# Optimization experiments

Measured on AMD Instinct MI355X. Metric: run time of the kernel, lower is better.

Reference implementation:

```python
import jax, jax.numpy as jnp
import numpy as np


def setup_inputs() -> dict:
    key = jax.random.key(0)
    k1, k2 = jax.random.split(key)
    B, T, D = 16, 4096, 512
    x = jax.random.normal(k1, (B, T, D), dtype=jnp.float32)
    alpha = jax.random.normal(k2, (1, 1, D), dtype=jnp.float32)  # raw param, pre-sigmoid
    return {"x": x, "alpha": alpha}


def reference(x, alpha):
    # s_0 = x_0 ; s_t = a * x_t + (1 - a) * s_{t-1}, a = sigmoid(alpha)
    a = jax.nn.sigmoid(alpha[0, 0, :])  # (D,)
    one_minus_a = 1.0 - a

    def step(prev, xt):  # prev, xt: (B, D)
        cur = a * xt + one_minus_a * prev
        return cur, cur

    x_t = jnp.swapaxes(x, 0, 1)  # (T, B, D)
    init = x_t[0]
    _, rest = jax.lax.scan(step, init, x_t[1:])  # (T-1, B, D)
    states = jnp.concatenate([x_t[:1], rest], axis=0)  # (T, B, D)
    return jnp.swapaxes(states, 0, 1)  # (B, T, D)
```

## Files before the change

kernel.cpp:

```cpp
#include <hip/hip_runtime.h>
#include <math.h>

#define BB 16
#define TT 4096
#define DD 512
#define D4 128

constexpr int CC = 256;
constexpr int LL = TT / CC;

typedef float floatx4 __attribute__((ext_vector_type(4)));

__device__ __forceinline__ float sigmf(float v) {
    return 1.0f / (1.0f + expf(-v));
}

__global__ __launch_bounds__(256) void es_chunk_ends(
    const float* __restrict__ x, const float* __restrict__ alpha,
    float* __restrict__ ends)
{
    const int c   = blockIdx.x;
    const int tid = threadIdx.x;
    const int b   = (blockIdx.y << 1) + (tid >> 7);
    const int d4  = tid & 127;

    const float4* xp = reinterpret_cast<const float4*>(x)
                     + ((size_t)b * TT + (size_t)c * LL) * D4 + d4;

    float4 v[LL];
    #pragma unroll
    for (int i = 0; i < LL; ++i) v[i] = xp[(size_t)i * D4];

    const float4 al = reinterpret_cast<const float4*>(alpha)[d4];
    const float ax = sigmf(al.x), ay = sigmf(al.y), az = sigmf(al.z), aw = sigmf(al.w);
    const float fx = 1.0f - ax, fy = 1.0f - ay, fz = 1.0f - az, fw = 1.0f - aw;

    float4 s;
    if (c == 0) {
        s = v[0];
    } else {
        s.x = s.y = s.z = s.w = 0.0f;
    }

    #pragma unroll
    for (int i = 0; i < LL; ++i) {
        s.x = fmaf(ax, v[i].x, fx * s.x);
        s.y = fmaf(ay, v[i].y, fy * s.y);
        s.z = fmaf(az, v[i].z, fz * s.z);
        s.w = fmaf(aw, v[i].w, fw * s.w);
    }

    reinterpret_cast<float4*>(ends)[((size_t)b * CC + c) * D4 + d4] = s;
}

__global__ __launch_bounds__(256) void es_carry_scan(
    float* __restrict__ ends, const float* __restrict__ alpha)
{
    const int g  = blockIdx.x * 256 + threadIdx.x;
    const int b  = g >> 7;
    const int d4 = g & 127;

    const float4 al = reinterpret_cast<const float4*>(alpha)[d4];
    const float ax = sigmf(al.x), ay = sigmf(al.y), az = sigmf(al.z), aw = sigmf(al.w);
    float4 fL;
    fL.x = powf(1.0f - ax, (float)LL);
    fL.y = powf(1.0f - ay, (float)LL);
    fL.z = powf(1.0f - az, (float)LL);
    fL.w = powf(1.0f - aw, (float)LL);

    float4* e = reinterpret_cast<float4*>(ends) + (size_t)b * CC * D4 + d4;

    constexpr int P = 16;
    float4 buf[P];
    #pragma unroll
    for (int j = 0; j < P; ++j) buf[j] = e[(size_t)(1 + j) * D4];

    float4 S = e[0];
    int c = 1;
    while (c + P <= CC) {
        #pragma unroll
        for (int j = 0; j < P; ++j) {
            const float4 v = buf[j];
            const int pf = c + P;
            if (pf < CC) buf[j] = e[(size_t)pf * D4];
            S.x = fmaf(fL.x, S.x, v.x);
            S.y = fmaf(fL.y, S.y, v.y);
            S.z = fmaf(fL.z, S.z, v.z);
            S.w = fmaf(fL.w, S.w, v.w);
            e[(size_t)c * D4] = S;
            ++c;
        }
    }
    for (int j = 0; c < CC; ++c, ++j) {
        const float4 v = buf[j];
        S.x = fmaf(fL.x, S.x, v.x);
        S.y = fmaf(fL.y, S.y, v.y);
        S.z = fmaf(fL.z, S.z, v.z);
        S.w = fmaf(fL.w, S.w, v.w);
        e[(size_t)c * D4] = S;
    }
}

__global__ __launch_bounds__(256) void es_final(
    const float* __restrict__ x, const float* __restrict__ alpha,
    const float* __restrict__ carries, float* __restrict__ out)
{
    const int c   = blockIdx.x;
    const int tid = threadIdx.x;
    const int b   = (blockIdx.y << 1) + (tid >> 7);
    const int d4  = tid & 127;

    float4 s;
    if (c != 0) {
        s = reinterpret_cast<const float4*>(carries)[((size_t)b * CC + (c - 1)) * D4 + d4];
    }

    const size_t base = ((size_t)b * TT + (size_t)c * LL) * D4 + d4;
    const float4* xp = reinterpret_cast<const float4*>(x) + base;
    floatx4*      op = reinterpret_cast<floatx4*>(out) + base;

    float4 v[LL];
    #pragma unroll
    for (int i = 0; i < LL; ++i) v[i] = xp[(size_t)i * D4];

    const float4 al = reinterpret_cast<const float4*>(alpha)[d4];
    const float ax = sigmf(al.x), ay = sigmf(al.y), az = sigmf(al.z), aw = sigmf(al.w);
    const float fx = 1.0f - ax, fy = 1.0f - ay, fz = 1.0f - az, fw = 1.0f - aw;

    if (c == 0) s = v[0];

    #pragma unroll
    for (int i = 0; i < LL; ++i) {
        s.x = fmaf(ax, v[i].x, fx * s.x);
        s.y = fmaf(ay, v[i].y, fy * s.y);
        s.z = fmaf(az, v[i].z, fz * s.z);
        s.w = fmaf(aw, v[i].w, fw * s.w);
        floatx4 sv = { s.x, s.y, s.z, s.w };
        __builtin_nontemporal_store(sv, op + (size_t)i * D4);
    }
}

__global__ __launch_bounds__(256) void es_serial(
    const float* __restrict__ x, const float* __restrict__ alpha,
    float* __restrict__ out)
{
    const int g  = blockIdx.x * 256 + threadIdx.x;
    const int b  = g >> 7;
    const int d4 = g & 127;

    const float4 al = reinterpret_cast<const float4*>(alpha)[d4];
    const float ax = sigmf(al.x), ay = sigmf(al.y), az = sigmf(al.z), aw = sigmf(al.w);
    const float fx = 1.0f - ax, fy = 1.0f - ay, fz = 1.0f - az, fw = 1.0f - aw;

    const float4* xp = reinterpret_cast<const float4*>(x) + (size_t)b * TT * D4 + d4;
    float4*       op = reinterpret_cast<float4*>(out) + (size_t)b * TT * D4 + d4;

    float4 s = xp[0];
    #pragma unroll 4
    for (int t = 0; t < TT; ++t) {
        const float4 v = xp[(size_t)t * D4];
        s.x = fmaf(ax, v.x, fx * s.x);
        s.y = fmaf(ay, v.y, fy * s.y);
        s.z = fmaf(az, v.z, fz * s.z);
        s.w = fmaf(aw, v.w, fw * s.w);
        op[(size_t)t * D4] = s;
    }
}

extern "C" void kernel_launch(void* const* d_in, const int* in_sizes, int n_in,
                              void* d_out, int out_size, void* d_ws, size_t ws_size,
                              hipStream_t stream)
{
    const float* x     = (const float*)d_in[0];
    const float* alpha = (const float*)d_in[1];
    float*       out   = (float*)d_out;

    const size_t need = (size_t)BB * CC * DD * sizeof(float);
    if (ws_size < need) {
        es_serial<<<dim3(8), 256, 0, stream>>>(x, alpha, out);
        return;
    }

    float* ends = (float*)d_ws;
    es_chunk_ends<<<dim3(CC, BB / 2), 256, 0, stream>>>(x, alpha, ends);
    es_carry_scan<<<dim3(8), 256, 0, stream>>>(ends, alpha);
    es_final<<<dim3(CC, BB / 2), 256, 0, stream>>>(x, alpha, ends, out);
}
```

Measured before the change: 270.8 us.

## Fuse three-pass chunked scan into one cooperative kernel with grid syncs

```diff
diff --git a/kernel.cpp b/kernel.cpp
--- a/kernel.cpp
+++ b/kernel.cpp
@@ -1,18 +1,141 @@
 #include <hip/hip_runtime.h>
+#include <hip/hip_cooperative_groups.h>
 #include <math.h>
+
+namespace cg = cooperative_groups;
 
 #define BB 16
 #define TT 4096
 #define DD 512
 #define D4 128
 
-constexpr int CC = 256;
-constexpr int LL = TT / CC;
+constexpr int CCF = 128;
+constexpr int LLF = TT / CCF;
+constexpr int CC  = 256;
+constexpr int LL  = TT / CC;
 
 typedef float floatx4 __attribute__((ext_vector_type(4)));
 
 __device__ __forceinline__ float sigmf(float v) {
     return 1.0f / (1.0f + expf(-v));
+}
+
+__global__ __launch_bounds__(256, 4) void es_fused(
+    const float* __restrict__ x, const float* __restrict__ alpha,
+    float* __restrict__ ends, float* __restrict__ out)
+{
+    const int tid = threadIdx.x;
+    const int c   = blockIdx.x & (CCF - 1);
+    const int b   = ((blockIdx.x >> 7) << 1) + (tid >> 7);
+    const int d4  = tid & 127;
+
+    const float4 al = reinterpret_cast<const float4*>(alpha)[d4];
+    const float ax = sigmf(al.x), ay = sigmf(al.y), az = sigmf(al.z), aw = sigmf(al.w);
+    const float fx = 1.0f - ax, fy = 1.0f - ay, fz = 1.0f - az, fw = 1.0f - aw;
+
+    const size_t base = ((size_t)b * TT + (size_t)c * LLF) * D4 + d4;
+
+    {
+        const float4* xp = reinterpret_cast<const float4*>(x) + base;
+        constexpr int W = 8;
+        float4 w[W];
+        #pragma unroll
+        for (int j = 0; j < W; ++j) w[j] = xp[(size_t)j * D4];
+
+        float4 s;
+        if (c == 0) s = w[0];
+        else        { s.x = s.y = s.z = s.w = 0.0f; }
+
+        #pragma unroll
+        for (int i = 0; i < LLF; ++i) {
+            const float4 v = w[i & (W - 1)];
+            if (i + W < LLF) w[i & (W - 1)] = xp[(size_t)(i + W) * D4];
+            s.x = fmaf(ax, v.x, fx * s.x);
+            s.y = fmaf(ay, v.y, fy * s.y);
+            s.z = fmaf(az, v.z, fz * s.z);
+            s.w = fmaf(aw, v.w, fw * s.w);
+        }
+        reinterpret_cast<float4*>(ends)[((size_t)b * CCF + c) * D4 + d4] = s;
+    }
+
+    cg::this_grid().sync();
+
+    {
+        const int g = blockIdx.x * 256 + tid;
+        if (g < BB * D4) {
+            const int sb  = g >> 7;
+            const int sd4 = g & 127;
+            const float4 sal = reinterpret_cast<const float4*>(alpha)[sd4];
+            float4 fL;
+            fL.x = powf(1.0f - sigmf(sal.x), (float)LLF);
+            fL.y = powf(1.0f - sigmf(sal.y), (float)LLF);
+            fL.z = powf(1.0f - sigmf(sal.z), (float)LLF);
+            fL.w = powf(1.0f - sigmf(sal.w), (float)LLF);
+
+            float4* e = reinterpret_cast<float4*>(ends) + (size_t)sb * CCF * D4 + sd4;
+
+            constexpr int P = 8;
+            float4 buf[P];
+            #pragma unroll
+            for (int j = 0; j < P; ++j) buf[j] = e[(size_t)(1 + j) * D4];
+
+            float4 S = e[0];
+            int cc = 1;
+            while (cc + P <= CCF) {
+                #pragma unroll
+                for (int j = 0; j < P; ++j) {
+                    const float4 v = buf[j];
+                    const int pf = cc + P;
+                    if (pf < CCF) buf[j] = e[(size_t)pf * D4];
+                    S.x = fmaf(fL.x, S.x, v.x);
+                    S.y = fmaf(fL.y, S.y, v.y);
+                    S.z = fmaf(fL.z, S.z, v.z);
+                    S.w = fmaf(fL.w, S.w, v.w);
+                    e[(size_t)cc * D4] = S;
+                    ++cc;
+                }
+            }
+            for (int j = 0; cc < CCF; ++cc, ++j) {
+                const float4 v = buf[j];
+                S.x = fmaf(fL.x, S.x, v.x);
+                S.y = fmaf(fL.y, S.y, v.y);
+                S.z = fmaf(fL.z, S.z, v.z);
+                S.w = fmaf(fL.w, S.w, v.w);
+                e[(size_t)cc * D4] = S;
+            }
+        }
+    }
+
+    cg::this_grid().sync();
+
+    {
+        const float4* xp = reinterpret_cast<const float4*>(x) + base;
+        asm volatile("" : "+v"(xp));
+        floatx4* op = reinterpret_cast<floatx4*>(out) + base;
+
+        float4 s;
+        if (c != 0) {
+            s = reinterpret_cast<const float4*>(ends)[((size_t)b * CCF + (c - 1)) * D4 + d4];
+        }
+
+        constexpr int W = 8;
+        float4 w[W];
+        #pragma unroll
+        for (int j = 0; j < W; ++j) w[j] = xp[(size_t)j * D4];
+        if (c == 0) s = w[0];
+
+        #pragma unroll
+        for (int i = 0; i < LLF; ++i) {
+            const float4 v = w[i & (W - 1)];
+            if (i + W < LLF) w[i & (W - 1)] = xp[(size_t)(i + W) * D4];
+            s.x = fmaf(ax, v.x, fx * s.x);
+            s.y = fmaf(ay, v.y, fy * s.y);
+            s.z = fmaf(az, v.z, fz * s.z);
+            s.w = fmaf(aw, v.w, fw * s.w);
+            floatx4 sv = { s.x, s.y, s.z, s.w };
+            __builtin_nontemporal_store(sv, op + (size_t)i * D4);
+        }
+    }
 }
 
 __global__ __launch_bounds__(256) void es_chunk_ends(
@@ -36,11 +159,8 @@
     const float fx = 1.0f - ax, fy = 1.0f - ay, fz = 1.0f - az, fw = 1.0f - aw;
 
     float4 s;
-    if (c == 0) {
-        s = v[0];
-    } else {
-        s.x = s.y = s.z = s.w = 0.0f;
-    }
+    if (c == 0) s = v[0];
+    else        { s.x = s.y = s.z = s.w = 0.0f; }
 
     #pragma unroll
     for (int i = 0; i < LL; ++i) {
@@ -49,7 +169,6 @@
         s.z = fmaf(az, v[i].z, fz * s.z);
         s.w = fmaf(aw, v[i].w, fw * s.w);
     }
-
     reinterpret_cast<float4*>(ends)[((size_t)b * CC + c) * D4 + d4] = s;
 }
 
@@ -61,12 +180,11 @@
     const int d4 = g & 127;
 
     const float4 al = reinterpret_cast<const float4*>(alpha)[d4];
-    const float ax = sigmf(al.x), ay = sigmf(al.y), az = sigmf(al.z), aw = sigmf(al.w);
     float4 fL;
-    fL.x = powf(1.0f - ax, (float)LL);
-    fL.y = powf(1.0f - ay, (float)LL);
-    fL.z = powf(1.0f - az, (float)LL);
-    fL.w = powf(1.0f - aw, (float)LL);
+    fL.x = powf(1.0f - sigmf(al.x), (float)LL);
+    fL.y = powf(1.0f - sigmf(al.y), (float)LL);
+    fL.z = powf(1.0f - sigmf(al.z), (float)LL);
+    fL.w = powf(1.0f - sigmf(al.w), (float)LL);
 
     float4* e = reinterpret_cast<float4*>(ends) + (size_t)b * CC * D4 + d4;
 
@@ -175,12 +293,23 @@
     const float* alpha = (const float*)d_in[1];
     float*       out   = (float*)d_out;
 
+    int coop = 0;
+    hipDeviceGetAttribute(&coop, hipDeviceAttributeCooperativeLaunch, 0);
+
+    const size_t need_f = (size_t)BB * CCF * DD * sizeof(float);
+    if (coop && ws_size >= need_f) {
+        float* ends = (float*)d_ws;
+        void* args[] = { (void*)&x, (void*)&alpha, (void*)&ends, (void*)&out };
+        hipError_t err = hipLaunchCooperativeKernel(
+            (const void*)es_fused, dim3(BB / 2 * CCF), dim3(256), args, 0, stream);
+        if (err == hipSuccess) return;
+    }
+
     const size_t need = (size_t)BB * CC * DD * sizeof(float);
     if (ws_size < need) {
         es_serial<<<dim3(8), 256, 0, stream>>>(x, alpha, out);
         return;
     }
-
     float* ends = (float*)d_ws;
     es_chunk_ends<<<dim3(CC, BB / 2), 256, 0, stream>>>(x, alpha, ends);
     es_carry_scan<<<dim3(8), 256, 0, stream>>>(ends, alpha);
```

Result: slower. 496.8 us (+83.4%).

## Fuse three-pass chunked scan into one block kernel with shared-memory carry scan

Applied to the files above, without the earlier changes.

```diff
diff --git a/kernel.cpp b/kernel.cpp
--- a/kernel.cpp
+++ b/kernel.cpp
@@ -6,8 +6,9 @@
 #define DD 512
 #define D4 128
 
-constexpr int CC = 256;
-constexpr int LL = TT / CC;
+constexpr int G   = 4;
+constexpr int NC  = 64;
+constexpr int LCH = TT / NC;
 
 typedef float floatx4 __attribute__((ext_vector_type(4)));
 
@@ -15,155 +16,99 @@
     return 1.0f / (1.0f + expf(-v));
 }
 
-__global__ __launch_bounds__(256) void es_chunk_ends(
+__global__ __launch_bounds__(256) void es_block(
     const float* __restrict__ x, const float* __restrict__ alpha,
-    float* __restrict__ ends)
+    float* __restrict__ out)
 {
-    const int c   = blockIdx.x;
     const int tid = threadIdx.x;
-    const int b   = (blockIdx.y << 1) + (tid >> 7);
-    const int d4  = tid & 127;
-
-    const float4* xp = reinterpret_cast<const float4*>(x)
-                     + ((size_t)b * TT + (size_t)c * LL) * D4 + d4;
-
-    float4 v[LL];
-    #pragma unroll
-    for (int i = 0; i < LL; ++i) v[i] = xp[(size_t)i * D4];
+    const int g   = tid & (G - 1);
+    const int tc  = tid >> 2;
+    const int b   = blockIdx.x >> 5;
+    const int grp = blockIdx.x & 31;
+    const int d4  = (grp << 2) + g;
 
     const float4 al = reinterpret_cast<const float4*>(alpha)[d4];
     const float ax = sigmf(al.x), ay = sigmf(al.y), az = sigmf(al.z), aw = sigmf(al.w);
     const float fx = 1.0f - ax, fy = 1.0f - ay, fz = 1.0f - az, fw = 1.0f - aw;
 
+    const size_t base = ((size_t)b * TT + (size_t)tc * LCH) * D4 + d4;
+    const float4* xp = reinterpret_cast<const float4*>(x) + base;
+
     float4 s;
-    if (c == 0) {
-        s = v[0];
-    } else {
-        s.x = s.y = s.z = s.w = 0.0f;
+    {
+        constexpr int W = 8;
+        float4 w[W];
+        #pragma unroll
+        for (int j = 0; j < W; ++j) w[j] = xp[(size_t)j * D4];
+        if (tc == 0) s = w[0];
+        else         { s.x = s.y = s.z = s.w = 0.0f; }
+        #pragma unroll
+        for (int i = 0; i < LCH; ++i) {
+            const float4 v = w[i & (W - 1)];
+            if (i + W < LCH) w[i & (W - 1)] = xp[(size_t)(i + W) * D4];
+            s.x = fmaf(ax, v.x, fx * s.x);
+            s.y = fmaf(ay, v.y, fy * s.y);
+            s.z = fmaf(az, v.z, fz * s.z);
+            s.w = fmaf(aw, v.w, fw * s.w);
+        }
     }
 
+    __shared__ float4 Eb[256];
+    float4 fp;
+    fp.x = fx; fp.y = fy; fp.z = fz; fp.w = fw;
     #pragma unroll
-    for (int i = 0; i < LL; ++i) {
-        s.x = fmaf(ax, v[i].x, fx * s.x);
-        s.y = fmaf(ay, v[i].y, fy * s.y);
-        s.z = fmaf(az, v[i].z, fz * s.z);
-        s.w = fmaf(aw, v[i].w, fw * s.w);
+    for (int k = 0; k < 6; ++k) {
+        fp.x *= fp.x; fp.y *= fp.y; fp.z *= fp.z; fp.w *= fp.w;
     }
 
-    reinterpret_cast<float4*>(ends)[((size_t)b * CC + c) * D4 + d4] = s;
-}
+    float4 S = s;
+    Eb[tid] = S;
+    #pragma unroll
+    for (int off = 1; off < NC; off <<= 1) {
+        __syncthreads();
+        float4 Sp;
+        const bool act = (tc >= off);
+        if (act) Sp = Eb[tid - off * G];
+        __syncthreads();
+        if (act) {
+            S.x = fmaf(fp.x, Sp.x, S.x);
+            S.y = fmaf(fp.y, Sp.y, S.y);
+            S.z = fmaf(fp.z, Sp.z, S.z);
+            S.w = fmaf(fp.w, Sp.w, S.w);
+        }
+        Eb[tid] = S;
+        fp.x *= fp.x; fp.y *= fp.y; fp.z *= fp.z; fp.w *= fp.w;
+    }
+    __syncthreads();
 
-__global__ __launch_bounds__(256) void es_carry_scan(
-    float* __restrict__ ends, const float* __restrict__ alpha)
-{
-    const int g  = blockIdx.x * 256 + threadIdx.x;
-    const int b  = g >> 7;
-    const int d4 = g & 127;
+    float4 carry;
+    if (tc > 0) carry = Eb[tid - G];
 
-    const float4 al = reinterpret_cast<const float4*>(alpha)[d4];
-    const float ax = sigmf(al.x), ay = sigmf(al.y), az = sigmf(al.z), aw = sigmf(al.w);
-    float4 fL;
-    fL.x = powf(1.0f - ax, (float)LL);
-    fL.y = powf(1.0f - ay, (float)LL);
-    fL.z = powf(1.0f - az, (float)LL);
-    fL.w = powf(1.0f - aw, (float)LL);
+    {
+        const float4* xq = xp;
+        asm volatile("" : "+v"(xq));
+        floatx4* op = reinterpret_cast<floatx4*>(out) + base;
 
-    float4* e = reinterpret_cast<float4*>(ends) + (size_t)b * CC * D4 + d4;
+        constexpr int W = 8;
+        float4 w[W];
+        #pragma unroll
+        for (int j = 0; j < W; ++j) w[j] = xq[(size_t)j * D4];
 
-    constexpr int P = 16;
-    float4 buf[P];
-    #pragma unroll
-    for (int j = 0; j < P; ++j) buf[j] = e[(size_t)(1 + j) * D4];
+        float4 t;
+        if (tc == 0) t = w[0];
+        else         t = carry;
 
-    float4 S = e[0];
-    int c = 1;
-    while (c + P <= CC) {
         #pragma unroll
-        for (int j = 0; j < P; ++j) {
-            const float4 v = buf[j];
-            const int pf = c + P;
-            if (pf < CC) buf[j] = e[(size_t)pf * D4];
-            S.x = fmaf(fL.x, S.x, v.x);
-            S.y = fmaf(fL.y, S.y, v.y);
-            S.z = fmaf(fL.z, S.z, v.z);
-            S.w = fmaf(fL.w, S.w, v.w);
-            e[(size_t)c * D4] = S;
-            ++c;
+        for (int i = 0; i < LCH; ++i) {
+            const float4 v = w[i & (W - 1)];
+            if (i + W < LCH) w[i & (W - 1)] = xq[(size_t)(i + W) * D4];
+            t.x = fmaf(ax, v.x, fx * t.x);
+            t.y = fmaf(ay, v.y, fy * t.y);
+            t.z = fmaf(az, v.z, fz * t.z);
+            t.w = fmaf(aw, v.w, fw * t.w);
+            floatx4 sv = { t.x, t.y, t.z, t.w };
+            __builtin_nontemporal_store(sv, op + (size_t)i * D4);
         }
-    }
-    for (int j = 0; c < CC; ++c, ++j) {
-        const float4 v = buf[j];
-        S.x = fmaf(fL.x, S.x, v.x);
-        S.y = fmaf(fL.y, S.y, v.y);
-        S.z = fmaf(fL.z, S.z, v.z);
-        S.w = fmaf(fL.w, S.w, v.w);
-        e[(size_t)c * D4] = S;
-    }
-}
-
-__global__ __launch_bounds__(256) void es_final(
-    const float* __restrict__ x, const float* __restrict__ alpha,
-    const float* __restrict__ carries, float* __restrict__ out)
-{
-    const int c   = blockIdx.x;
-    const int tid = threadIdx.x;
-    const int b   = (blockIdx.y << 1) + (tid >> 7);
-    const int d4  = tid & 127;
-
-    float4 s;
-    if (c != 0) {
-        s = reinterpret_cast<const float4*>(carries)[((size_t)b * CC + (c - 1)) * D4 + d4];
-    }
-
-    const size_t base = ((size_t)b * TT + (size_t)c * LL) * D4 + d4;
-    const float4* xp = reinterpret_cast<const float4*>(x) + base;
-    floatx4*      op = reinterpret_cast<floatx4*>(out) + base;
-
-    float4 v[LL];
-    #pragma unroll
-    for (int i = 0; i < LL; ++i) v[i] = xp[(size_t)i * D4];
-
-    const float4 al = reinterpret_cast<const float4*>(alpha)[d4];
-    const float ax = sigmf(al.x), ay = sigmf(al.y), az = sigmf(al.z), aw = sigmf(al.w);
-    const float fx = 1.0f - ax, fy = 1.0f - ay, fz = 1.0f - az, fw = 1.0f - aw;
-
-    if (c == 0) s = v[0];
-
-    #pragma unroll
-    for (int i = 0; i < LL; ++i) {
-        s.x = fmaf(ax, v[i].x, fx * s.x);
-        s.y = fmaf(ay, v[i].y, fy * s.y);
-        s.z = fmaf(az, v[i].z, fz * s.z);
-        s.w = fmaf(aw, v[i].w, fw * s.w);
-        floatx4 sv = { s.x, s.y, s.z, s.w };
-        __builtin_nontemporal_store(sv, op + (size_t)i * D4);
-    }
-}
-
-__global__ __launch_bounds__(256) void es_serial(
-    const float* __restrict__ x, const float* __restrict__ alpha,
-    float* __restrict__ out)
-{
-    const int g  = blockIdx.x * 256 + threadIdx.x;
-    const int b  = g >> 7;
-    const int d4 = g & 127;
-
-    const float4 al = reinterpret_cast<const float4*>(alpha)[d4];
-    const float ax = sigmf(al.x), ay = sigmf(al.y), az = sigmf(al.z), aw = sigmf(al.w);
-    const float fx = 1.0f - ax, fy = 1.0f - ay, fz = 1.0f - az, fw = 1.0f - aw;
-
-    const float4* xp = reinterpret_cast<const float4*>(x) + (size_t)b * TT * D4 + d4;
-    float4*       op = reinterpret_cast<float4*>(out) + (size_t)b * TT * D4 + d4;
-
-    float4 s = xp[0];
-    #pragma unroll 4
-    for (int t = 0; t < TT; ++t) {
-        const float4 v = xp[(size_t)t * D4];
-        s.x = fmaf(ax, v.x, fx * s.x);
-        s.y = fmaf(ay, v.y, fy * s.y);
-        s.z = fmaf(az, v.z, fz * s.z);
-        s.w = fmaf(aw, v.w, fw * s.w);
-        op[(size_t)t * D4] = s;
     }
 }
 
@@ -174,15 +119,7 @@
     const float* x     = (const float*)d_in[0];
     const float* alpha = (const float*)d_in[1];
     float*       out   = (float*)d_out;
+    (void)d_ws; (void)ws_size;
 
-    const size_t need = (size_t)BB * CC * DD * sizeof(float);
-    if (ws_size < need) {
-        es_serial<<<dim3(8), 256, 0, stream>>>(x, alpha, out);
-        return;
-    }
-
-    float* ends = (float*)d_ws;
-    es_chunk_ends<<<dim3(CC, BB / 2), 256, 0, stream>>>(x, alpha, ends);
-    es_carry_scan<<<dim3(8), 256, 0, stream>>>(ends, alpha);
-    es_final<<<dim3(CC, BB / 2), 256, 0, stream>>>(x, alpha, ends, out);
+    es_block<<<dim3(BB * 32), 256, 0, stream>>>(x, alpha, out);
 }
```

Measured after the change: 293.4 us. +8.3%, slower.
